# Performance work log

Hardware: AMD Instinct MI355X
Metric: run time of the kernel (lower is better)

## Reference

```python
import jax, jax.numpy as jnp
import numpy as np

# Malvar-He-Cutler demosaic kernels: 4 output feature maps from the 1-channel bayer mosaic.
_K = [
    0, 0, -2, 0, 0,  0, 0, 4, 0, 0,  -2, 4, 8, 4, -2,  0, 0, 4, 0, 0,  0, 0, -2, 0, 0,
    0, 0, -3, 0, 0,  0, 4, 0, 4, 0,  -3, 0, 12, 0, -3,  0, 4, 0, 4, 0,  0, 0, -3, 0, 0,
    0, 0, 1, 0, 0,  0, -2, 0, -2, 0,  -2, 8, 10, 8, -2,  0, -2, 0, -2, 0,  0, 0, 1, 0, 0,
    0, 0, -2, 0, 0,  0, -2, 8, -2, 0,  1, 0, 10, 0, 1,  0, -2, 8, -2, 0,  0, 0, -2, 0, 0,
]
KERNELS = jnp.asarray(np.asarray(_K, dtype=np.float32).reshape(4, 1, 5, 5) / 16.0)
# Per-output-channel (R,G,B), per-quadrant (2x2) source channel into feats=(conv4 || x) -> 5 channels.
INDICES_RGGB = np.array([4, 2, 3, 1, 0, 4, 4, 0, 1, 3, 2, 4]).reshape(1, 3, 2, 2)


def _calc_index(pattern):
    p = tuple(np.asarray(pattern).flatten().tolist())
    if p == (0, 1, 1, 2):
        return INDICES_RGGB
    if p == (1, 0, 2, 1):
        return np.roll(INDICES_RGGB, 1, axis=-1)
    if p == (1, 2, 0, 1):
        return np.roll(INDICES_RGGB, 1, axis=-2)
    if p == (2, 1, 1, 0):
        return np.roll(np.roll(INDICES_RGGB, 1, axis=-1), 1, axis=-2)
    raise ValueError('Invalid bayer pattern')


def _pixel_shuffle(x, r):
    N, C, H, W = x.shape
    c = C // (r * r)
    return x.reshape(N, c, r, r, H, W).transpose(0, 1, 4, 2, 5, 3).reshape(N, c, H * r, W * r)


def _gather_bayer(x, index):
    """x: (N, C_in, H, W); index: (1|N, C_out, 2, 2) -> (N, C_out, H, W).
    Efficient equivalent of the original one-hot mask multiply-sum: a direct
    per-quadrant channel selection via take_along_axis."""
    N, C, H, W = x.shape
    iN, Cout = index.shape[0], index.shape[1]
    h, w = H // 2, W // 2
    # pixel_unshuffle(x,2) with channel order c*4 + (2*i + j): quadrant axis q.
    xq = x.reshape(N, C, h, 2, w, 2).transpose(0, 1, 3, 5, 2, 4).reshape(N, C, 4, h, w)
    xq = xq.swapaxes(1, 2)  # (N, 4, C, h, w)
    iq = index.reshape(iN, Cout, 4).swapaxes(1, 2)  # (iN, 4, Cout)
    iq = jnp.broadcast_to(iq, (N, 4, Cout))
    gath = jnp.take_along_axis(xq, iq[:, :, :, None, None], axis=2)  # (N, 4, Cout, h, w)
    y_down = gath.swapaxes(1, 2).reshape(N, Cout * 4, h, w)
    return _pixel_shuffle(y_down, 2)


def setup_inputs() -> dict:
    key = jax.random.key(0)
    x = jax.random.uniform(key, (16, 1, 1024, 1024), dtype=jnp.float32)
    bayer_pattern = jnp.array([0, 1, 1, 2], dtype=jnp.int64 if jax.config.jax_enable_x64 else jnp.int32).reshape(1, 1, 2, 2)  # RGGB
    return {"x": x, "bayer_pattern": bayer_pattern}


def reference(x, bayer_pattern) -> jnp.ndarray:
    # Replication pad by 2 on each side, then 5x5 conv producing 4 feature maps.
    x_pad = jnp.pad(x, ((0, 0), (0, 0), (2, 2), (2, 2)), mode='edge')
    feats = jax.lax.conv_general_dilated(
        x_pad, KERNELS.astype(x.dtype), window_strides=(1, 1), padding='VALID',
        dimension_numbers=('NCHW', 'OIHW', 'NCHW'))
    feats = jnp.concatenate([feats, x], axis=1)  # (N, 5, H, W)
    bp = np.asarray(bayer_pattern)  # bayer pattern is static metadata
    index = jnp.asarray(np.concatenate([_calc_index(bp[n]) for n in range(bp.shape[0])], axis=0))
    return _gather_bayer(feats, index)  # (N, 3, H, W)
```

## Files before the change

### kernel.cpp

```cpp
#include <hip/hip_runtime.h>


constexpr int H = 1024, W = 1024;
constexpr int TILE_W = 256, TILE_H = 64;
constexpr int RPT = 16;

typedef float v4f __attribute__((ext_vector_type(4)));

__global__ __launch_bounds__(256, 4) void demosaic_kernel(
    const float* __restrict__ xin_all, const int* __restrict__ bp,
    float* __restrict__ out)
{
    const int tx = threadIdx.x;
    const int ty = threadIdx.y;
    const int x0 = blockIdx.x * TILE_W;
    const int n  = blockIdx.z;
    const int gx = x0 + tx * 4;
    const int ry0 = blockIdx.y * TILE_H + ty * RPT;

    const int p0 = bp[0], p1 = bp[1];
    const int fi = (p0 == 2) || (p0 == 1 && p1 == 2);
    const int fj = (p0 == 2) || (p0 == 1 && p1 == 0);

    const float* __restrict__ xin = xin_all + (size_t)n * H * W;

    const bool lfix = (gx == 0);
    const bool rfix = (gx == W - 4);
    const int xl = lfix ? 0  : gx - 4;
    const int xr = rfix ? gx : gx + 4;

    float w[5][8];

    auto LOADROW = [&](int gy, v4f& L, v4f& M, v4f& R) {
        gy = min(max(gy, 0), H - 1);
        const float* row = xin + (size_t)gy * W;
        L = *(const v4f*)(row + xl);
        M = *(const v4f*)(row + gx);
        R = *(const v4f*)(row + xr);
    };
    auto INSERT = [&](float (&d)[8], v4f L, v4f M, v4f R) {
        d[0] = lfix ? M.x : L.z;
        d[1] = lfix ? M.x : L.w;
        d[2] = M.x; d[3] = M.y; d[4] = M.z; d[5] = M.w;
        d[6] = rfix ? M.w : R.x;
        d[7] = rfix ? M.w : R.y;
    };

    {
        v4f L[5], M[5], R[5];
        #pragma unroll
        for (int m = 0; m < 5; ++m) LOADROW(ry0 - 2 + m, L[m], M[m], R[m]);
        #pragma unroll
        for (int m = 0; m < 5; ++m) INSERT(w[m], L[m], M[m], R[m]);
    }

    #pragma unroll
    for (int dr = 0; dr < RPT; ++dr) {
        v4f Lp, Mp, Rp;
        if (dr < RPT - 1) LOADROW(ry0 + dr + 3, Lp, Mp, Rp);

        #define WR_(m) (w[(dr + (m)) % 5])
        const int qi = (dr & 1) ^ fi;

        float r4[4], g4[4], b4[4];
        #pragma unroll
        for (int p = 0; p < 4; ++p) {
            const float c   = WR_(2)[p + 2];
            const float up  = WR_(1)[p + 2], dn  = WR_(3)[p + 2];
            const float lf  = WR_(2)[p + 1], rt  = WR_(2)[p + 3];
            const float up2 = WR_(0)[p + 2], dn2 = WR_(4)[p + 2];
            const float lf2 = WR_(2)[p + 0], rt2 = WR_(2)[p + 4];
            const float dg  = WR_(1)[p + 1] + WR_(1)[p + 3]
                            + WR_(3)[p + 1] + WR_(3)[p + 3];

            const float axH = lf2 + rt2;
            const float axV = up2 + dn2;
            const float ax  = axH + axV;
            const float crossHV = (up + dn) + (lf + rt);

            const float s0 = (8.0f  * c + 4.0f * crossHV   - 2.0f * ax) * 0.0625f;
            const float s1 = (12.0f * c + 4.0f * dg        - 3.0f * ax) * 0.0625f;
            const float s2 = (10.0f * c + 8.0f * (lf + rt) - 2.0f * (axH + dg) + axV) * 0.0625f;
            const float s3 = (10.0f * c + 8.0f * (up + dn) - 2.0f * (axV + dg) + axH) * 0.0625f;

            const int qj = (p & 1) ^ fj;
            const int qt = (qi << 1) | qj;
            r4[p] = (qt == 0) ? c  : (qt == 1) ? s2 : (qt == 2) ? s3 : s1;
            g4[p] = (qi == qj) ? s0 : c;
            b4[p] = (qt == 0) ? s1 : (qt == 1) ? s3 : (qt == 2) ? s2 : c;
        }
        #undef WR_

        const int y = ry0 + dr;
        const size_t rowoff = (size_t)y * W + gx;
        v4f* const oR = (v4f*)(out + (size_t)(n * 3 + 0) * H * W + rowoff);
        v4f* const oG = (v4f*)(out + (size_t)(n * 3 + 1) * H * W + rowoff);
        v4f* const oB = (v4f*)(out + (size_t)(n * 3 + 2) * H * W + rowoff);
        v4f vR = { r4[0], r4[1], r4[2], r4[3] };
        v4f vG = { g4[0], g4[1], g4[2], g4[3] };
        v4f vB = { b4[0], b4[1], b4[2], b4[3] };
        __builtin_nontemporal_store(vR, oR);
        __builtin_nontemporal_store(vG, oG);
        __builtin_nontemporal_store(vB, oB);

        if (dr < RPT - 1) INSERT(w[dr % 5], Lp, Mp, Rp);
    }
}

extern "C" void kernel_launch(void* const* d_in, const int* in_sizes, int n_in,
                              void* d_out, int out_size, void* d_ws, size_t ws_size,
                              hipStream_t stream) {
    const float* x  = (const float*)d_in[0];
    const int*   bp = (const int*)d_in[1];
    float* out = (float*)d_out;
    const int N = in_sizes[0] / (H * W);
    dim3 grid(W / TILE_W, H / TILE_H, N);
    dim3 block(64, 4, 1);
    demosaic_kernel<<<grid, block, 0, stream>>>(x, bp, out);
}
```

Measured before the change: 253.8 us.

## Load all stencil rows upfront with unaligned loads and shrink per-thread rows

Each thread now computes 4 output rows instead of 16. It loads all 8 needed input rows at once using two unaligned 16-byte loads per row, instead of streaming a rolling 5-row window with three aligned loads per row. The grid grows fourfold and the occupancy hint is removed. The aim is more memory-level parallelism and fewer load instructions, at the cost of more redundant halo reads and misaligned accesses.

```diff
diff --git a/kernel.cpp b/kernel.cpp
--- a/kernel.cpp
+++ b/kernel.cpp
@@ -2,21 +2,19 @@
 
 
 constexpr int H = 1024, W = 1024;
-constexpr int TILE_W = 256, TILE_H = 64;
-constexpr int RPT = 16;
 
-typedef float v4f __attribute__((ext_vector_type(4)));
+typedef float v4f  __attribute__((ext_vector_type(4)));
+typedef float v4fu __attribute__((ext_vector_type(4), aligned(4)));
 
-__global__ __launch_bounds__(256, 4) void demosaic_kernel(
+__global__ __launch_bounds__(256) void demosaic_kernel(
     const float* __restrict__ xin_all, const int* __restrict__ bp,
     float* __restrict__ out)
 {
-    const int tx = threadIdx.x;
-    const int ty = threadIdx.y;
-    const int x0 = blockIdx.x * TILE_W;
-    const int n  = blockIdx.z;
-    const int gx = x0 + tx * 4;
-    const int ry0 = blockIdx.y * TILE_H + ty * RPT;
+    const int tx  = threadIdx.x;
+    const int ty  = threadIdx.y;
+    const int gx  = blockIdx.x * 256 + tx * 4;
+    const int ry0 = blockIdx.y * 16  + ty * 4;
+    const int n   = blockIdx.z;
 
     const int p0 = bp[0], p1 = bp[1];
     const int fi = (p0 == 2) || (p0 == 1 && p1 == 2);
@@ -26,52 +24,45 @@
 
     const bool lfix = (gx == 0);
     const bool rfix = (gx == W - 4);
-    const int xl = lfix ? 0  : gx - 4;
-    const int xr = rfix ? gx : gx + 4;
+    const int  xa = lfix ? gx : gx - 2;
+    const int  xb = rfix ? gx : gx + 2;
 
-    float w[5][8];
+    v4f A[8], B[8];
+    #pragma unroll
+    for (int r = 0; r < 8; ++r) {
+        const int gy = min(max(ry0 - 2 + r, 0), H - 1);
+        const float* row = xin + (size_t)gy * W;
+        A[r] = *(const v4fu*)(row + xa);
+        B[r] = *(const v4fu*)(row + xb);
+    }
 
-    auto LOADROW = [&](int gy, v4f& L, v4f& M, v4f& R) {
-        gy = min(max(gy, 0), H - 1);
-        const float* row = xin + (size_t)gy * W;
-        L = *(const v4f*)(row + xl);
-        M = *(const v4f*)(row + gx);
-        R = *(const v4f*)(row + xr);
-    };
-    auto INSERT = [&](float (&d)[8], v4f L, v4f M, v4f R) {
-        d[0] = lfix ? M.x : L.z;
-        d[1] = lfix ? M.x : L.w;
-        d[2] = M.x; d[3] = M.y; d[4] = M.z; d[5] = M.w;
-        d[6] = rfix ? M.w : R.x;
-        d[7] = rfix ? M.w : R.y;
-    };
-
-    {
-        v4f L[5], M[5], R[5];
-        #pragma unroll
-        for (int m = 0; m < 5; ++m) LOADROW(ry0 - 2 + m, L[m], M[m], R[m]);
-        #pragma unroll
-        for (int m = 0; m < 5; ++m) INSERT(w[m], L[m], M[m], R[m]);
+    float w[8][8];
+    #pragma unroll
+    for (int r = 0; r < 8; ++r) {
+        w[r][0] = A[r].x;
+        w[r][1] = lfix ? A[r].x : A[r].y;
+        w[r][2] = lfix ? A[r].x : A[r].z;
+        w[r][3] = lfix ? A[r].y : A[r].w;
+        w[r][4] = rfix ? B[r].z : B[r].x;
+        w[r][5] = rfix ? B[r].w : B[r].y;
+        w[r][6] = rfix ? B[r].w : B[r].z;
+        w[r][7] = B[r].w;
     }
 
     #pragma unroll
-    for (int dr = 0; dr < RPT; ++dr) {
-        v4f Lp, Mp, Rp;
-        if (dr < RPT - 1) LOADROW(ry0 + dr + 3, Lp, Mp, Rp);
-
-        #define WR_(m) (w[(dr + (m)) % 5])
+    for (int dr = 0; dr < 4; ++dr) {
         const int qi = (dr & 1) ^ fi;
 
         float r4[4], g4[4], b4[4];
         #pragma unroll
         for (int p = 0; p < 4; ++p) {
-            const float c   = WR_(2)[p + 2];
-            const float up  = WR_(1)[p + 2], dn  = WR_(3)[p + 2];
-            const float lf  = WR_(2)[p + 1], rt  = WR_(2)[p + 3];
-            const float up2 = WR_(0)[p + 2], dn2 = WR_(4)[p + 2];
-            const float lf2 = WR_(2)[p + 0], rt2 = WR_(2)[p + 4];
-            const float dg  = WR_(1)[p + 1] + WR_(1)[p + 3]
-                            + WR_(3)[p + 1] + WR_(3)[p + 3];
+            const float c   = w[dr + 2][p + 2];
+            const float up  = w[dr + 1][p + 2], dn  = w[dr + 3][p + 2];
+            const float lf  = w[dr + 2][p + 1], rt  = w[dr + 2][p + 3];
+            const float up2 = w[dr + 0][p + 2], dn2 = w[dr + 4][p + 2];
+            const float lf2 = w[dr + 2][p + 0], rt2 = w[dr + 2][p + 4];
+            const float dg  = w[dr + 1][p + 1] + w[dr + 1][p + 3]
+                            + w[dr + 3][p + 1] + w[dr + 3][p + 3];
 
             const float axH = lf2 + rt2;
             const float axV = up2 + dn2;
@@ -89,7 +80,6 @@
             g4[p] = (qi == qj) ? s0 : c;
             b4[p] = (qt == 0) ? s1 : (qt == 1) ? s3 : (qt == 2) ? s2 : c;
         }
-        #undef WR_
 
         const int y = ry0 + dr;
         const size_t rowoff = (size_t)y * W + gx;
@@ -102,8 +92,6 @@
         __builtin_nontemporal_store(vR, oR);
         __builtin_nontemporal_store(vG, oG);
         __builtin_nontemporal_store(vB, oB);
-
-        if (dr < RPT - 1) INSERT(w[dr % 5], Lp, Mp, Rp);
     }
 }
 
@@ -114,7 +102,7 @@
     const int*   bp = (const int*)d_in[1];
     float* out = (float*)d_out;
     const int N = in_sizes[0] / (H * W);
-    dim3 grid(W / TILE_W, H / TILE_H, N);
+    dim3 grid(W / 256, H / 16, N);
     dim3 block(64, 4, 1);
     demosaic_kernel<<<grid, block, 0, stream>>>(x, bp, out);
 }
```

Result: faster. 247.3 us (-2.5%).
